# Kernel optimization log

Measured on AMD Instinct MI355X. Metric: run time of the kernel, lower is better.

The kernel has to match this reference:

```python
import jax, jax.numpy as jnp
import numpy as np

NEG_SLOPE = 0.2  # PyG GATConv leaky_relu slope


def gat_conv(x, src, dst, W, a_src, a_dst, bias, heads, out_ch, concat, n_nodes):
    # x: [N, in], W: [heads*out_ch, in], a_src/a_dst: [heads, out_ch]
    h = (x @ W.T).reshape(n_nodes, heads, out_ch)          # [N,H,C]
    alpha_src = (h * a_src).sum(-1)                         # [N,H]
    alpha_dst = (h * a_dst).sum(-1)                         # [N,H]
    e = jax.nn.leaky_relu(alpha_src[src] + alpha_dst[dst], NEG_SLOPE)  # [E,H]
    # segment softmax over incoming edges of each dst node (self-loops ensure non-empty)
    m = jax.ops.segment_max(e, dst, num_segments=n_nodes)
    e = jnp.exp(e - m[dst])
    s = jax.ops.segment_sum(e, dst, num_segments=n_nodes)
    alpha = e / (s[dst] + 1e-16)                            # [E,H]
    msg = h[src] * alpha[:, :, None]                        # [E,H,C]
    out = jax.ops.segment_sum(msg, dst, num_segments=n_nodes)  # [N,H,C]
    out = out.reshape(n_nodes, heads * out_ch) if concat else out.mean(axis=1)
    return out + bias


def setup_inputs() -> dict:
    key = jax.random.key(0)
    ks = jax.random.split(key, 16)
    N, E, IN, HID, OUT, H1, H2 = 10000, 160000, 256, 32, 32, 8, 10
    inp = {
        "x": jax.random.normal(ks[0], (N, IN), dtype=jnp.float32),
        "edge_index": jax.random.randint(ks[1], (2, E), 0, N, dtype=jnp.int64),
        # GATConv 1: in=256 -> 8 heads x 32
        "W1": jax.random.normal(ks[2], (H1 * HID, IN), dtype=jnp.float32) * 0.05,
        "a1s": jax.random.normal(ks[3], (H1, HID), dtype=jnp.float32) * 0.05,
        "a1d": jax.random.normal(ks[4], (H1, HID), dtype=jnp.float32) * 0.05,
        "b1": jnp.zeros((H1 * HID,), dtype=jnp.float32),
        # GATConv 2: in=256 -> 8 heads x 32
        "W2": jax.random.normal(ks[5], (H1 * HID, H1 * HID), dtype=jnp.float32) * 0.05,
        "a2s": jax.random.normal(ks[6], (H1, HID), dtype=jnp.float32) * 0.05,
        "a2d": jax.random.normal(ks[7], (H1, HID), dtype=jnp.float32) * 0.05,
        "b2": jnp.zeros((H1 * HID,), dtype=jnp.float32),
        # GATConv 3: in=256 -> 10 heads x 32, concat=False (mean)
        "W3": jax.random.normal(ks[8], (H2 * OUT, H1 * HID), dtype=jnp.float32) * 0.05,
        "a3s": jax.random.normal(ks[9], (H2, OUT), dtype=jnp.float32) * 0.05,
        "a3d": jax.random.normal(ks[10], (H2, OUT), dtype=jnp.float32) * 0.05,
        "b3": jnp.zeros((OUT,), dtype=jnp.float32),
        # residual projections
        "P1W": jax.random.normal(ks[11], (H1 * HID, IN), dtype=jnp.float32) * 0.05,
        "P1b": jnp.zeros((H1 * HID,), dtype=jnp.float32),
        "P3W": jax.random.normal(ks[12], (OUT, H1 * HID), dtype=jnp.float32) * 0.05,
        "P3b": jnp.zeros((OUT,), dtype=jnp.float32),
    }
    return inp


def reference(x, edge_index, W1, a1s, a1d, b1, W2, a2s, a2d, b2,
              W3, a3s, a3d, b3, P1W, P1b, P3W, P3b):
    N = x.shape[0]
    loop = jnp.arange(N, dtype=edge_index.dtype)
    src = jnp.concatenate([edge_index[0], loop])  # PyG adds self-loops by default
    dst = jnp.concatenate([edge_index[1], loop])

    identity1 = x @ P1W.T + P1b
    h = gat_conv(x, src, dst, W1, a1s, a1d, b1, 8, 32, True, N)
    h = jax.nn.elu(h) + identity1  # dropout inactive in eval

    identity2 = h
    h2 = gat_conv(h, src, dst, W2, a2s, a2d, b2, 8, 32, True, N)
    h = jax.nn.elu(h2) + identity2

    identity3 = h @ P3W.T + P3b
    h3 = gat_conv(h, src, dst, W3, a3s, a3d, b3, 10, 32, False, N)
    return h3 + identity3
```

## Files before the change

kernel.cpp:

```cpp
#include <hip/hip_runtime.h>
#include <hip/hip_bf16.h>

typedef __hip_bfloat16 bf16;
typedef __attribute__((ext_vector_type(8))) short bf16x8;
typedef __attribute__((ext_vector_type(4))) short bf16x4;
typedef __attribute__((ext_vector_type(4))) float f32x4;


static __device__ __forceinline__ float bf2f(bf16 v) { return __bfloat162float(v); }
static __device__ __forceinline__ float bf2fs(short v) {
    unsigned int u = ((unsigned int)(unsigned short)v) << 16;
    return __builtin_bit_cast(float, u);
}
static __device__ __forceinline__ short f2bfs(float f) {
    bf16 b = __float2bfloat16(f);
    return __builtin_bit_cast(short, b);
}
static __device__ __forceinline__ float loadf(const void* p, size_t i, int isf32) {
    return isf32 ? ((const float*)p)[i] : bf2f(((const bf16*)p)[i]);
}
static __device__ __forceinline__ int get_isf32(const int* flags) {
    return (flags[0] | (flags[2] == 0)) ? 1 : 0;
}
static __device__ __forceinline__ void wave_lds_fence() {
    asm volatile("s_waitcnt lgkmcnt(0)" ::: "memory");
}

__global__ void k_zero(int* __restrict__ flags, int* __restrict__ cnt, int N) {
    int i = blockIdx.x * blockDim.x + threadIdx.x;
    if (i < 4) flags[i] = 0;
    for (; i < N; i += gridDim.x * blockDim.x) cnt[i] = 0;
}

__global__ void k_detect(const unsigned short* __restrict__ xu, const int* __restrict__ ew,
                         int* __restrict__ flags, int nx, int ne2, int bx) {
    __shared__ int lf[3];
    if (threadIdx.x < 3) lf[threadIdx.x] = 0;
    __syncthreads();
    if ((int)blockIdx.x < bx) {
        for (int i = blockIdx.x * 256 + threadIdx.x; i < nx; i += bx * 256) {
            unsigned short v = xu[i];
            if ((v & 0x7F80u) == 0x7F80u) lf[0] = 1;
            if (((i & 1) == 0) && v != 0) lf[2] = 1;
        }
    } else {
        int nb = gridDim.x - bx;
        for (int i = (blockIdx.x - bx) * 256 + threadIdx.x; i < ne2; i += nb * 256) {
            if ((i & 1) && ew[i] != 0) lf[1] = 1;
        }
    }
    __syncthreads();
    if (threadIdx.x == 0) {
        if (lf[0]) atomicOr(&flags[0], 1);
        if (lf[1]) atomicOr(&flags[1], 1);
        if (lf[2]) atomicOr(&flags[2], 1);
    }
}

static __device__ __forceinline__ void cast8(const void* src, bf16* dst, int i8, int isf32) {
    if (isf32) {
        f32x4 a = ((const f32x4*)src)[2 * i8];
        f32x4 b = ((const f32x4*)src)[2 * i8 + 1];
        bf16x8 o;
        o[0] = f2bfs(a[0]); o[1] = f2bfs(a[1]); o[2] = f2bfs(a[2]); o[3] = f2bfs(a[3]);
        o[4] = f2bfs(b[0]); o[5] = f2bfs(b[1]); o[6] = f2bfs(b[2]); o[7] = f2bfs(b[3]);
        ((bf16x8*)dst)[i8] = o;
    } else {
        ((bf16x8*)dst)[i8] = ((const bf16x8*)src)[i8];
    }
}

__global__ void k_cast_norm(const void* s0, bf16* d0, int c0,
                            const void* s1, bf16* d1, int c1,
                            const void* s2, bf16* d2, int c2,
                            const void* s3, bf16* d3, int c3,
                            const void* s4, bf16* d4, int c4,
                            const void* s5, bf16* d5, int c5,
                            const int* __restrict__ w, int* __restrict__ es,
                            int* __restrict__ ed, int* __restrict__ cnt, int E,
                            const int* __restrict__ flags, int cb) {
    if ((int)blockIdx.x < cb) {
        int t = blockIdx.x * 256 + threadIdx.x;
        int isf32 = get_isf32(flags);
        if (t < c0) { if (isf32) cast8(s0, d0, t, 1); return; } t -= c0;
        if (t < c1) { cast8(s1, d1, t, isf32); return; } t -= c1;
        if (t < c2) { cast8(s2, d2, t, isf32); return; } t -= c2;
        if (t < c3) { cast8(s3, d3, t, isf32); return; } t -= c3;
        if (t < c4) { cast8(s4, d4, t, isf32); return; } t -= c4;
        if (t < c5) { cast8(s5, d5, t, isf32); }
    } else {
        int e = (blockIdx.x - cb) * 256 + threadIdx.x;
        if (e >= E) return;
        int sv, dv;
        if (flags[1] == 0) {
            sv = w[2 * (size_t)e];
            dv = w[2 * (size_t)E + 2 * (size_t)e];
        } else {
            sv = w[e];
            dv = w[(size_t)E + e];
        }
        es[e] = sv;
        ed[e] = dv;
        atomicAdd(&cnt[dv], 1);
    }
}

__global__ void k_scan(int* __restrict__ cnt, int* __restrict__ row_ptr, int N) {
    __shared__ int part[1024];
    int tid = threadIdx.x;
    int vpt = (N + 1023) >> 10;
    int i0 = tid * vpt;
    int i1 = i0 + vpt; if (i1 > N) i1 = N;
    int s = 0;
    for (int i = i0; i < i1; ++i) s += cnt[i] + 1;
    part[tid] = s;
    __syncthreads();
    for (int off = 1; off < 1024; off <<= 1) {
        int t = (tid >= off) ? part[tid - off] : 0;
        __syncthreads();
        part[tid] += t;
        __syncthreads();
    }
    int run = (tid == 0) ? 0 : part[tid - 1];
    for (int i = i0; i < i1; ++i) {
        int c = cnt[i] + 1;
        cnt[i] = run;
        run += c;
        row_ptr[i + 1] = run;
    }
    if (tid == 0) row_ptr[0] = 0;
}

__global__ void k_fill(const int* __restrict__ edst, int* __restrict__ cursor,
                       const int* __restrict__ row_ptr, int* __restrict__ csr_e,
                       int E, int N) {
    int e = blockIdx.x * blockDim.x + threadIdx.x;
    if (e < E) {
        int d = edst[e];
        int pos = atomicAdd(&cursor[d], 1);
        csr_e[pos] = e;
    } else if (e < E + N) {
        int d = e - E;
        csr_e[row_ptr[d + 1] - 1] = e;
    }
}

template<int NT, int KK>
__global__ void k_gemm_split(const bf16* __restrict__ Acast, const void* __restrict__ Araw,
                             const bf16* __restrict__ W,
                             const void* __restrict__ bias1, const int* __restrict__ flags,
                             bf16* __restrict__ out0, int S0, int ld0,
                             bf16* __restrict__ out1, int ld1, int n1,
                             int M, int Fo,
                             const void* __restrict__ aS, const void* __restrict__ aD,
                             float* __restrict__ asrc, float* __restrict__ adst, int H) {
    int wid = threadIdx.x >> 6;
    int lane = threadIdx.x & 63;
    int mrow = blockIdx.x * 64 + wid * 16;
    if (mrow >= M) return;
    int isf32 = get_isf32(flags);
    const bf16* A = (Araw && !isf32) ? (const bf16*)Araw : Acast;
    int ncol = blockIdx.y * (NT * 16);
    int r = lane & 15, g = lane >> 4;

    f32x4 acc[NT];
#pragma unroll
    for (int t = 0; t < NT; ++t) acc[t] = (f32x4){0.f, 0.f, 0.f, 0.f};

    const bf16* arow = A + (size_t)(mrow + r) * KK + g * 8;
    const bf16* wbase = W + (size_t)(ncol + r) * KK + g * 8;
#pragma unroll
    for (int k0 = 0; k0 < KK; k0 += 32) {
        bf16x8 af = *(const bf16x8*)(arow + k0);
#pragma unroll
        for (int t = 0; t < NT; ++t) {
            bf16x8 bfr = *(const bf16x8*)(wbase + (size_t)t * 16 * KK + k0);
            acc[t] = __builtin_amdgcn_mfma_f32_16x16x32_bf16(af, bfr, acc[t], 0, 0, 0);
        }
    }

#pragma unroll
    for (int t = 0; t < NT; ++t) {
        int n = ncol + t * 16 + r;
        bool is0 = n < S0;
        int jc = n - S0;
        float bv = (!is0 && jc < n1 && bias1) ? loadf(bias1, jc, isf32) : 0.f;
#pragma unroll
        for (int j = 0; j < 4; ++j) {
            int m = mrow + 4 * g + j;
            float v = acc[t][j] + bv;
            if (is0) out0[(size_t)m * ld0 + n] = __float2bfloat16(v);
            else if (jc < n1) out1[(size_t)m * ld1 + jc] = __float2bfloat16(v);
        }
    }

    if (aS && ncol < S0) {
        float ps[2][4], pd[2][4];
#pragma unroll
        for (int hb = 0; hb < 2; ++hb)
#pragma unroll
            for (int j = 0; j < 4; ++j) { ps[hb][j] = 0.f; pd[hb][j] = 0.f; }
#pragma unroll
        for (int t = 0; t < NT; ++t) {
            int col = ncol + t * 16 + r;
            float asv = loadf(aS, col, isf32);
            float adv = loadf(aD, col, isf32);
#pragma unroll
            for (int j = 0; j < 4; ++j) {
                ps[t >> 1][j] += acc[t][j] * asv;
                pd[t >> 1][j] += acc[t][j] * adv;
            }
        }
#pragma unroll
        for (int mk = 1; mk <= 8; mk <<= 1) {
#pragma unroll
            for (int hb = 0; hb < 2; ++hb)
#pragma unroll
                for (int j = 0; j < 4; ++j) {
                    ps[hb][j] += __shfl_xor(ps[hb][j], mk);
                    pd[hb][j] += __shfl_xor(pd[hb][j], mk);
                }
        }
        if (r == 0) {
            int hA = ncol >> 5, hB = hA + 1;
#pragma unroll
            for (int j = 0; j < 4; ++j) {
                int m = mrow + 4 * g + j;
                asrc[(size_t)m * H + hA] = ps[0][j];
                asrc[(size_t)m * H + hB] = ps[1][j];
                adst[(size_t)m * H + hA] = pd[0][j];
                adst[(size_t)m * H + hB] = pd[1][j];
            }
        }
    }
}

#define CAP 96
__global__ void k_fused_agg(const bf16* __restrict__ hlin,
                            const float* __restrict__ asrc, const float* __restrict__ adst,
                            const int* __restrict__ esrc, const int* __restrict__ row_ptr,
                            const int* __restrict__ csr_e,
                            const void* __restrict__ bias, const bf16* __restrict__ identb,
                            void* __restrict__ out, bf16* __restrict__ outb,
                            const int* __restrict__ flags,
                            int E, int N, int H, int mode) {
    __shared__ float el[4][CAP * 10];
    __shared__ int   ssrc[4][CAP];
    __shared__ float idn[4][10];
    int wid = threadIdx.x >> 6, lane = threadIdx.x & 63;
    int d = blockIdx.x * 4 + wid;
    bool active = d < N;
    int isf32 = get_isf32(flags);
    int F = H * 32;
    int nj = (F + 255) >> 8;
    int lo = 0, deg = 0;
    if (active) { lo = row_ptr[d]; deg = row_ptr[d + 1] - lo; }
    bool fast = deg <= CAP;
    if (!active) return;

    if (fast) {
        int EC = 64 / H;
        int h = lane % H, ei = lane / H;
        float ad = adst[(size_t)d * H + h];
        for (int base = 0; base < deg; base += EC) {
            int p = base + ei;
            if (ei < EC && p < deg) {
                int e = csr_e[lo + p];
                int s = (e < E) ? esrc[e] : (e - E);
                float v = asrc[(size_t)s * H + h] + ad;
                v = (v > 0.f) ? v : 0.2f * v;
                el[wid][p * H + h] = v;
                if (h == 0) ssrc[wid][p] = s;
            }
        }
    }
    wave_lds_fence();
    if (fast) {
        if (H == 8) {
            int h = lane & 7, sub = lane >> 3;
            float m = -1e30f;
            for (int p = sub; p < deg; p += 8) m = fmaxf(m, el[wid][p * 8 + h]);
            m = fmaxf(m, __shfl_xor(m, 8));
            m = fmaxf(m, __shfl_xor(m, 16));
            m = fmaxf(m, __shfl_xor(m, 32));
            float den = 0.f;
            for (int p = sub; p < deg; p += 8) {
                float t = __expf(el[wid][p * 8 + h] - m);
                el[wid][p * 8 + h] = t;
                den += t;
            }
            den += __shfl_xor(den, 8);
            den += __shfl_xor(den, 16);
            den += __shfl_xor(den, 32);
            if (lane < 8) idn[wid][lane] = 1.f / (den + 1e-16f);
        } else if (lane < H) {
            float m = -1e30f;
            for (int p = 0; p < deg; ++p) m = fmaxf(m, el[wid][p * H + lane]);
            float den = 0.f;
            for (int p = 0; p < deg; ++p) {
                float t = __expf(el[wid][p * H + lane] - m);
                el[wid][p * H + lane] = t;
                den += t;
            }
            idn[wid][lane] = 1.f / (den + 1e-16f);
        }
    }
    wave_lds_fence();

    if (mode == 1 && fast) {
        int g = lane & 15, q = lane >> 4;
        int f0 = g * 16;
        f32x4 a0 = {0.f,0.f,0.f,0.f}, a1 = {0.f,0.f,0.f,0.f};
        f32x4 a2 = {0.f,0.f,0.f,0.f}, a3 = {0.f,0.f,0.f,0.f};
        int p = q;
        for (; p + 4 < deg; p += 8) {
            int s0 = ssrc[wid][p];
            int s1 = ssrc[wid][p + 4];
            const bf16* hp0 = hlin + (size_t)s0 * 256 + f0;
            const bf16* hp1 = hlin + (size_t)s1 * 256 + f0;
            bf16x8 u0 = *(const bf16x8*)hp0;
            bf16x8 u1 = *(const bf16x8*)(hp0 + 8);
            bf16x8 v0 = *(const bf16x8*)hp1;
            bf16x8 v1 = *(const bf16x8*)(hp1 + 8);
            float w0 = el[wid][p * 8 + (g >> 1)];
            float w1 = el[wid][(p + 4) * 8 + (g >> 1)];
#pragma unroll
            for (int k = 0; k < 4; ++k) {
                a0[k] += w0 * bf2fs(u0[k]);
                a1[k] += w0 * bf2fs(u0[4 + k]);
                a2[k] += w0 * bf2fs(u1[k]);
                a3[k] += w0 * bf2fs(u1[4 + k]);
                a0[k] += w1 * bf2fs(v0[k]);
                a1[k] += w1 * bf2fs(v0[4 + k]);
                a2[k] += w1 * bf2fs(v1[k]);
                a3[k] += w1 * bf2fs(v1[4 + k]);
            }
        }
        if (p < deg) {
            int s0 = ssrc[wid][p];
            const bf16* hp0 = hlin + (size_t)s0 * 256 + f0;
            bf16x8 u0 = *(const bf16x8*)hp0;
            bf16x8 u1 = *(const bf16x8*)(hp0 + 8);
            float w0 = el[wid][p * 8 + (g >> 1)];
#pragma unroll
            for (int k = 0; k < 4; ++k) {
                a0[k] += w0 * bf2fs(u0[k]);
                a1[k] += w0 * bf2fs(u0[4 + k]);
                a2[k] += w0 * bf2fs(u1[k]);
                a3[k] += w0 * bf2fs(u1[4 + k]);
            }
        }
#pragma unroll
        for (int k = 0; k < 4; ++k) {
            a0[k] += __shfl_xor(a0[k], 16); a1[k] += __shfl_xor(a1[k], 16);
            a2[k] += __shfl_xor(a2[k], 16); a3[k] += __shfl_xor(a3[k], 16);
            a0[k] += __shfl_xor(a0[k], 32); a1[k] += __shfl_xor(a1[k], 32);
            a2[k] += __shfl_xor(a2[k], 32); a3[k] += __shfl_xor(a3[k], 32);
        }
        if (lane < 16) {
            float inv = idn[wid][g >> 1];
            const bf16* idp = identb + (size_t)d * 256 + f0;
            bf16x8 id0 = *(const bf16x8*)idp;
            bf16x8 id1 = *(const bf16x8*)(idp + 8);
            bf16* ob = outb + (size_t)d * 256 + f0;
            f32x4 av[4] = {a0, a1, a2, a3};
            bf16x8 obv0, obv1;
#pragma unroll
            for (int i = 0; i < 4; ++i) {
#pragma unroll
                for (int k = 0; k < 4; ++k) {
                    float v = av[i][k] * inv + loadf(bias, f0 + 4 * i + k, isf32);
                    v = (v > 0.f) ? v : (__expf(v) - 1.f);
                    int e8 = 4 * i + k;
                    v += bf2fs((e8 < 8) ? id0[e8] : id1[e8 - 8]);
                    if (i < 2) obv0[e8] = f2bfs(v);
                    else       obv1[e8 - 8] = f2bfs(v);
                }
            }
            *(bf16x8*)ob = obv0;
            *(bf16x8*)(ob + 8) = obv1;
        }
        return;
    }

    if (mode == 2 && fast) {
        int g = lane & 15, q = lane >> 4;
        int f0 = g * 16;
        int f1 = 256 + g * 4;
        f32x4 a0 = {0.f,0.f,0.f,0.f}, a1 = {0.f,0.f,0.f,0.f};
        f32x4 a2 = {0.f,0.f,0.f,0.f}, a3 = {0.f,0.f,0.f,0.f};
        f32x4 a4 = {0.f,0.f,0.f,0.f};
        int p = q;
        for (; p + 4 < deg; p += 8) {
            int s0 = ssrc[wid][p];
            int s1 = ssrc[wid][p + 4];
            const bf16* hp0 = hlin + (size_t)s0 * 320;
            const bf16* hp1 = hlin + (size_t)s1 * 320;
            bf16x8 u0 = *(const bf16x8*)(hp0 + f0);
            bf16x8 u1 = *(const bf16x8*)(hp0 + f0 + 8);
            bf16x4 u2 = *(const bf16x4*)(hp0 + f1);
            bf16x8 v0 = *(const bf16x8*)(hp1 + f0);
            bf16x8 v1 = *(const bf16x8*)(hp1 + f0 + 8);
            bf16x4 v2 = *(const bf16x4*)(hp1 + f1);
            float w00 = el[wid][p * 10 + (g >> 1)];
            float w02 = el[wid][p * 10 + 8 + (g >> 3)];
            float w10 = el[wid][(p + 4) * 10 + (g >> 1)];
            float w12 = el[wid][(p + 4) * 10 + 8 + (g >> 3)];
#pragma unroll
            for (int k = 0; k < 4; ++k) {
                a0[k] += w00 * bf2fs(u0[k]);
                a1[k] += w00 * bf2fs(u0[4 + k]);
                a2[k] += w00 * bf2fs(u1[k]);
                a3[k] += w00 * bf2fs(u1[4 + k]);
                a4[k] += w02 * bf2fs(u2[k]);
                a0[k] += w10 * bf2fs(v0[k]);
                a1[k] += w10 * bf2fs(v0[4 + k]);
                a2[k] += w10 * bf2fs(v1[k]);
                a3[k] += w10 * bf2fs(v1[4 + k]);
                a4[k] += w12 * bf2fs(v2[k]);
            }
        }
        if (p < deg) {
            int s0 = ssrc[wid][p];
            const bf16* hp0 = hlin + (size_t)s0 * 320;
            bf16x8 u0 = *(const bf16x8*)(hp0 + f0);
            bf16x8 u1 = *(const bf16x8*)(hp0 + f0 + 8);
            bf16x4 u2 = *(const bf16x4*)(hp0 + f1);
            float w00 = el[wid][p * 10 + (g >> 1)];
            float w02 = el[wid][p * 10 + 8 + (g >> 3)];
#pragma unroll
            for (int k = 0; k < 4; ++k) {
                a0[k] += w00 * bf2fs(u0[k]);
                a1[k] += w00 * bf2fs(u0[4 + k]);
                a2[k] += w00 * bf2fs(u1[k]);
                a3[k] += w00 * bf2fs(u1[4 + k]);
                a4[k] += w02 * bf2fs(u2[k]);
            }
        }
#pragma unroll
        for (int k = 0; k < 4; ++k) {
            a0[k] += __shfl_xor(a0[k], 16); a1[k] += __shfl_xor(a1[k], 16);
            a2[k] += __shfl_xor(a2[k], 16); a3[k] += __shfl_xor(a3[k], 16);
            a4[k] += __shfl_xor(a4[k], 16);
            a0[k] += __shfl_xor(a0[k], 32); a1[k] += __shfl_xor(a1[k], 32);
            a2[k] += __shfl_xor(a2[k], 32); a3[k] += __shfl_xor(a3[k], 32);
            a4[k] += __shfl_xor(a4[k], 32);
        }
        float* scratch = &el[wid][0];
        if (lane < 16) {
            float inv0 = idn[wid][g >> 1];
            float inv2 = idn[wid][8 + (g >> 3)];
#pragma unroll
            for (int k = 0; k < 4; ++k) {
                scratch[f0 + k]      = a0[k] * inv0;
                scratch[f0 + 4 + k]  = a1[k] * inv0;
                scratch[f0 + 8 + k]  = a2[k] * inv0;
                scratch[f0 + 12 + k] = a3[k] * inv0;
                scratch[f1 + k]      = a4[k] * inv2;
            }
        }
        wave_lds_fence();
        if (lane < 32) {
            float s = 0.f;
#pragma unroll
            for (int h = 0; h < 10; ++h) s += scratch[h * 32 + lane];
            float v = s * 0.1f + loadf(bias, lane, isf32)
                    + bf2f(identb[(size_t)d * 32 + lane]);
            if (isf32) ((float*)out)[(size_t)d * 32 + lane] = v;
            else ((bf16*)out)[(size_t)d * 32 + lane] = __float2bfloat16(v);
        }
        return;
    }

    f32x4 acc[2] = {(f32x4){0.f,0.f,0.f,0.f}, (f32x4){0.f,0.f,0.f,0.f}};
    for (int j = 0; j < nj; ++j) {
        int f0 = (lane + 64 * j) * 4;
        if (f0 >= F) continue;
        int hj = f0 >> 5;
        float ad = adst[(size_t)d * H + hj];
        float m = -1e30f;
        for (int p = 0; p < deg; ++p) {
            int e = csr_e[lo + p];
            int s = (e < E) ? esrc[e] : (e - E);
            float v = asrc[(size_t)s * H + hj] + ad;
            v = (v > 0.f) ? v : 0.2f * v;
            m = fmaxf(m, v);
        }
        float den = 0.f;
        f32x4 a4 = {0.f, 0.f, 0.f, 0.f};
        for (int p = 0; p < deg; ++p) {
            int e = csr_e[lo + p];
            int s = (e < E) ? esrc[e] : (e - E);
            float v = asrc[(size_t)s * H + hj] + ad;
            v = (v > 0.f) ? v : 0.2f * v;
            float t = __expf(v - m);
            den += t;
            bf16x4 hv = *(const bf16x4*)(hlin + (size_t)s * F + f0);
            for (int k = 0; k < 4; ++k) a4[k] += t * bf2fs(hv[k]);
        }
        float inv = 1.f / (den + 1e-16f);
        for (int k = 0; k < 4; ++k) acc[j][k] = a4[k] * inv;
    }
    if (mode == 1) {
        int f0 = lane * 4;
        bf16x4 ob;
#pragma unroll
        for (int k = 0; k < 4; ++k) {
            float v = acc[0][k] + loadf(bias, f0 + k, isf32);
            v = (v > 0.f) ? v : (__expf(v) - 1.f);
            v += bf2f(identb[(size_t)d * F + f0 + k]);
            ob[k] = f2bfs(v);
        }
        *(bf16x4*)(outb + (size_t)d * F + f0) = ob;
    } else {
        float* scratch = &el[wid][0];
#pragma unroll
        for (int j = 0; j < 2; ++j) {
            int f0 = (lane + 64 * j) * 4;
            if (j < nj && f0 < F) {
#pragma unroll
                for (int k = 0; k < 4; ++k) scratch[f0 + k] = acc[j][k];
            }
        }
        wave_lds_fence();
        if (lane < 32) {
            float s = 0.f;
            for (int h = 0; h < H; ++h) s += scratch[h * 32 + lane];
            float v = s * (1.f / (float)H) + loadf(bias, lane, isf32)
                    + bf2f(identb[(size_t)d * 32 + lane]);
            if (isf32) ((float*)out)[(size_t)d * 32 + lane] = v;
            else ((bf16*)out)[(size_t)d * 32 + lane] = __float2bfloat16(v);
        }
    }
}

extern "C" void kernel_launch(void* const* d_in, const int* in_sizes, int n_in,
                              void* d_out, int out_size, void* d_ws, size_t ws_size,
                              hipStream_t stream) {
    const int IN = 256, C = 32;
    const int N = in_sizes[0] / IN;
    const int E = in_sizes[1] / 2;
    const int ET = E + N;

    const void* x    = d_in[0];
    const int*  edge = (const int*)d_in[1];
    const void* W1 = d_in[2];
    const void* a1s = d_in[3];
    const void* a1d = d_in[4];
    const void* b1 = d_in[5];
    const void* W2 = d_in[6];
    const void* a2s = d_in[7];
    const void* a2d = d_in[8];
    const void* b2 = d_in[9];
    const void* W3 = d_in[10];
    const void* a3s = d_in[11];
    const void* a3d = d_in[12];
    const void* b3 = d_in[13];
    const void* P1W = d_in[14];
    const void* P1b = d_in[15];
    const void* P3W = d_in[16];
    const void* P3b = d_in[17];

    char* ws = (char*)d_ws;
    size_t off = 0;
    auto alloc = [&](size_t bytes) -> void* {
        void* p = ws + off;
        off = (off + bytes + 255) & ~(size_t)255;
        return p;
    };
    bf16* fxb   = (bf16*)alloc((size_t)N * 256 * 2);
    bf16* fyb   = (bf16*)alloc((size_t)N * 256 * 2);
    bf16* fhb   = (bf16*)alloc((size_t)N * 320 * 2);
    bf16* fidb  = (bf16*)alloc((size_t)N * 256 * 2);
    float* fasrc = (float*)alloc((size_t)N * 10 * 4);
    float* fadst = (float*)alloc((size_t)N * 10 * 4);
    bf16* wc1   = (bf16*)alloc((size_t)512 * 256 * 2);
    bf16* wb2   = (bf16*)alloc((size_t)256 * 256 * 2);
    bf16* wc3   = (bf16*)alloc((size_t)384 * 256 * 2);
    int*  isrc  = (int*)alloc((size_t)E * 4);
    int*  idst  = (int*)alloc((size_t)E * 4);
    int*  irow  = (int*)alloc((size_t)(N + 1) * 4);
    int*  icur  = (int*)alloc((size_t)N * 4);
    int*  icsr  = (int*)alloc((size_t)ET * 4);
    int*  flags = (int*)alloc(4 * 4);
    (void)ws_size;

    auto cdiv = [](int a, int b) { return (a + b - 1) / b; };

    k_zero<<<cdiv(N, 256), 256, 0, stream>>>(flags, icur, N);

    int nprobe_x = (N * 256 < 16384) ? N * 256 : 16384;
    int nprobe_e = (2 * E < 8192) ? 2 * E : 8192;
    int bx = cdiv(nprobe_x, 256) < 16 ? cdiv(nprobe_x, 256) : 16;
    int be = cdiv(nprobe_e, 256) < 8 ? cdiv(nprobe_e, 256) : 8;
    k_detect<<<bx + be, 256, 0, stream>>>(
        (const unsigned short*)x, edge, flags, nprobe_x, nprobe_e, bx);

    int c_x = N * 256 / 8, c_w = 256 * 256 / 8, c_w3 = 320 * 256 / 8, c_p3 = 32 * 256 / 8;
    int ctot = c_x + 3 * c_w + c_w3 + c_p3;
    int cb = cdiv(ctot, 256);
    k_cast_norm<<<cb + cdiv(E, 256), 256, 0, stream>>>(
        x, fxb, c_x,
        W1, wc1, c_w,
        P1W, wc1 + (size_t)256 * 256, c_w,
        W2, wb2, c_w,
        W3, wc3, c_w3,
        P3W, wc3 + (size_t)320 * 256, c_p3,
        edge, isrc, idst, icur, E, flags, cb);

    k_scan<<<1, 1024, 0, stream>>>(icur, irow, N);
    k_fill<<<cdiv(ET, 256), 256, 0, stream>>>(idst, icur, irow, icsr, E, N);

    int gx = cdiv(N, 64);
    int ga = cdiv(N, 4);

    {
        int H = 8;
        k_gemm_split<4, 256><<<dim3(gx, 8), 256, 0, stream>>>(
            fxb, x, wc1, P1b, flags, fhb, 256, 256, fidb, 256, 256, N, 512,
            a1s, a1d, fasrc, fadst, H);
        k_fused_agg<<<ga, 256, 0, stream>>>(fhb, fasrc, fadst, isrc, irow, icsr,
                                            b1, fidb, nullptr, fyb, flags, E, N, H, 1);
    }
    {
        int H = 8;
        k_gemm_split<4, 256><<<dim3(gx, 4), 256, 0, stream>>>(
            fyb, nullptr, wb2, nullptr, flags, fhb, 256, 256, nullptr, 0, 0, N, 256,
            a2s, a2d, fasrc, fadst, H);
        k_fused_agg<<<ga, 256, 0, stream>>>(fhb, fasrc, fadst, isrc, irow, icsr,
                                            b2, fyb, nullptr, fyb, flags, E, N, H, 1);
    }
    {
        int H = 10;
        k_gemm_split<4, 256><<<dim3(gx, 6), 256, 0, stream>>>(
            fyb, nullptr, wc3, P3b, flags, fhb, 320, 320, fidb, 32, 32, N, 384,
            a3s, a3d, fasrc, fadst, H);
        k_fused_agg<<<ga, 256, 0, stream>>>(fhb, fasrc, fadst, isrc, irow, icsr,
                                            b3, fidb, d_out, nullptr, flags, E, N, H, 2);
    }
}
```

Before: 199.2 us.

## Widen GEMM column tile to 128 and read bf16 weights directly

Each GEMM block now covers 8 MFMA column tiles instead of 4, which halves the grid's y dimension and lets each A fragment be reused across twice as many columns. Weights are read through per-tile pointers into separate segment buffers, so bf16 inputs are used directly without a copy and the cast kernel exits early when the inputs are not fp32. The attention-score epilogue is generalized to handle more heads per block, with a boundary guard for the layer 3 split. The trade-off is higher register pressure from 8 accumulators and 8 weight pointers, plus fewer blocks in flight.

```diff
diff --git a/kernel.cpp b/kernel.cpp
--- a/kernel.cpp
+++ b/kernel.cpp
@@ -57,17 +57,13 @@
     }
 }
 
-static __device__ __forceinline__ void cast8(const void* src, bf16* dst, int i8, int isf32) {
-    if (isf32) {
-        f32x4 a = ((const f32x4*)src)[2 * i8];
-        f32x4 b = ((const f32x4*)src)[2 * i8 + 1];
-        bf16x8 o;
-        o[0] = f2bfs(a[0]); o[1] = f2bfs(a[1]); o[2] = f2bfs(a[2]); o[3] = f2bfs(a[3]);
-        o[4] = f2bfs(b[0]); o[5] = f2bfs(b[1]); o[6] = f2bfs(b[2]); o[7] = f2bfs(b[3]);
-        ((bf16x8*)dst)[i8] = o;
-    } else {
-        ((bf16x8*)dst)[i8] = ((const bf16x8*)src)[i8];
-    }
+static __device__ __forceinline__ void cast8(const void* src, bf16* dst, int i8) {
+    f32x4 a = ((const f32x4*)src)[2 * i8];
+    f32x4 b = ((const f32x4*)src)[2 * i8 + 1];
+    bf16x8 o;
+    o[0] = f2bfs(a[0]); o[1] = f2bfs(a[1]); o[2] = f2bfs(a[2]); o[3] = f2bfs(a[3]);
+    o[4] = f2bfs(b[0]); o[5] = f2bfs(b[1]); o[6] = f2bfs(b[2]); o[7] = f2bfs(b[3]);
+    ((bf16x8*)dst)[i8] = o;
 }
 
 __global__ void k_cast_norm(const void* s0, bf16* d0, int c0,
@@ -80,14 +76,14 @@
                             int* __restrict__ ed, int* __restrict__ cnt, int E,
                             const int* __restrict__ flags, int cb) {
     if ((int)blockIdx.x < cb) {
+        if (!get_isf32(flags)) return;
         int t = blockIdx.x * 256 + threadIdx.x;
-        int isf32 = get_isf32(flags);
-        if (t < c0) { if (isf32) cast8(s0, d0, t, 1); return; } t -= c0;
-        if (t < c1) { cast8(s1, d1, t, isf32); return; } t -= c1;
-        if (t < c2) { cast8(s2, d2, t, isf32); return; } t -= c2;
-        if (t < c3) { cast8(s3, d3, t, isf32); return; } t -= c3;
-        if (t < c4) { cast8(s4, d4, t, isf32); return; } t -= c4;
-        if (t < c5) { cast8(s5, d5, t, isf32); }
+        if (t < c0) { cast8(s0, d0, t); return; } t -= c0;
+        if (t < c1) { cast8(s1, d1, t); return; } t -= c1;
+        if (t < c2) { cast8(s2, d2, t); return; } t -= c2;
+        if (t < c3) { cast8(s3, d3, t); return; } t -= c3;
+        if (t < c4) { cast8(s4, d4, t); return; } t -= c4;
+        if (t < c5) { cast8(s5, d5, t); }
     } else {
         int e = (blockIdx.x - cb) * 256 + threadIdx.x;
         if (e >= E) return;
@@ -146,14 +142,16 @@
 }
 
 template<int NT, int KK>
-__global__ void k_gemm_split(const bf16* __restrict__ Acast, const void* __restrict__ Araw,
-                             const bf16* __restrict__ W,
-                             const void* __restrict__ bias1, const int* __restrict__ flags,
-                             bf16* __restrict__ out0, int S0, int ld0,
-                             bf16* __restrict__ out1, int ld1, int n1,
-                             int M, int Fo,
-                             const void* __restrict__ aS, const void* __restrict__ aD,
-                             float* __restrict__ asrc, float* __restrict__ adst, int H) {
+__global__ __launch_bounds__(256) void k_gemm_split(
+        const bf16* __restrict__ Acast, const void* __restrict__ Araw,
+        const void* __restrict__ W0raw, const bf16* __restrict__ W0cast, int S0,
+        const void* __restrict__ W1raw, const bf16* __restrict__ W1cast, int n1,
+        const void* __restrict__ bias1, const int* __restrict__ flags,
+        bf16* __restrict__ out0, int ld0,
+        bf16* __restrict__ out1, int ld1,
+        int M,
+        const void* __restrict__ aS, const void* __restrict__ aD,
+        float* __restrict__ asrc, float* __restrict__ adst, int H) {
     int wid = threadIdx.x >> 6;
     int lane = threadIdx.x & 63;
     int mrow = blockIdx.x * 64 + wid * 16;
@@ -163,18 +161,29 @@
     int ncol = blockIdx.y * (NT * 16);
     int r = lane & 15, g = lane >> 4;
 
+    const bf16* wptr[NT];
+#pragma unroll
+    for (int t = 0; t < NT; ++t) {
+        int nl = ncol + t * 16 + r;
+        bool is0 = nl < S0;
+        int jc = nl - S0;
+        int wr = is0 ? nl : ((jc < n1) ? jc : (n1 > 0 ? n1 - 1 : 0));
+        const bf16* wseg = is0 ? (isf32 ? W0cast : (const bf16*)W0raw)
+                               : (isf32 ? W1cast : (const bf16*)W1raw);
+        wptr[t] = wseg + (size_t)wr * KK + g * 8;
+    }
+
     f32x4 acc[NT];
 #pragma unroll
     for (int t = 0; t < NT; ++t) acc[t] = (f32x4){0.f, 0.f, 0.f, 0.f};
 
     const bf16* arow = A + (size_t)(mrow + r) * KK + g * 8;
-    const bf16* wbase = W + (size_t)(ncol + r) * KK + g * 8;
-#pragma unroll
+#pragma unroll 2
     for (int k0 = 0; k0 < KK; k0 += 32) {
         bf16x8 af = *(const bf16x8*)(arow + k0);
 #pragma unroll
         for (int t = 0; t < NT; ++t) {
-            bf16x8 bfr = *(const bf16x8*)(wbase + (size_t)t * 16 * KK + k0);
+            bf16x8 bfr = *(const bf16x8*)(wptr[t] + k0);
             acc[t] = __builtin_amdgcn_mfma_f32_16x16x32_bf16(af, bfr, acc[t], 0, 0, 0);
         }
     }
@@ -195,26 +204,28 @@
     }
 
     if (aS && ncol < S0) {
-        float ps[2][4], pd[2][4];
-#pragma unroll
-        for (int hb = 0; hb < 2; ++hb)
+        float ps[NT / 2][4], pd[NT / 2][4];
+#pragma unroll
+        for (int hb = 0; hb < NT / 2; ++hb)
 #pragma unroll
             for (int j = 0; j < 4; ++j) { ps[hb][j] = 0.f; pd[hb][j] = 0.f; }
 #pragma unroll
         for (int t = 0; t < NT; ++t) {
             int col = ncol + t * 16 + r;
-            float asv = loadf(aS, col, isf32);
-            float adv = loadf(aD, col, isf32);
-#pragma unroll
-            for (int j = 0; j < 4; ++j) {
-                ps[t >> 1][j] += acc[t][j] * asv;
-                pd[t >> 1][j] += acc[t][j] * adv;
+            if (col < S0) {
+                float asv = loadf(aS, col, isf32);
+                float adv = loadf(aD, col, isf32);
+#pragma unroll
+                for (int j = 0; j < 4; ++j) {
+                    ps[t >> 1][j] += acc[t][j] * asv;
+                    pd[t >> 1][j] += acc[t][j] * adv;
+                }
             }
         }
 #pragma unroll
         for (int mk = 1; mk <= 8; mk <<= 1) {
 #pragma unroll
-            for (int hb = 0; hb < 2; ++hb)
+            for (int hb = 0; hb < NT / 2; ++hb)
 #pragma unroll
                 for (int j = 0; j < 4; ++j) {
                     ps[hb][j] += __shfl_xor(ps[hb][j], mk);
@@ -222,14 +233,17 @@
                 }
         }
         if (r == 0) {
-            int hA = ncol >> 5, hB = hA + 1;
-#pragma unroll
-            for (int j = 0; j < 4; ++j) {
-                int m = mrow + 4 * g + j;
-                asrc[(size_t)m * H + hA] = ps[0][j];
-                asrc[(size_t)m * H + hB] = ps[1][j];
-                adst[(size_t)m * H + hA] = pd[0][j];
-                adst[(size_t)m * H + hB] = pd[1][j];
+#pragma unroll
+            for (int hb = 0; hb < NT / 2; ++hb) {
+                if (ncol + hb * 32 < S0) {
+                    int hA = (ncol >> 5) + hb;
+#pragma unroll
+                    for (int j = 0; j < 4; ++j) {
+                        int m = mrow + 4 * g + j;
+                        asrc[(size_t)m * H + hA] = ps[hb][j];
+                        adst[(size_t)m * H + hA] = pd[hb][j];
+                    }
+                }
             }
         }
     }
@@ -574,9 +588,11 @@
     bf16* fidb  = (bf16*)alloc((size_t)N * 256 * 2);
     float* fasrc = (float*)alloc((size_t)N * 10 * 4);
     float* fadst = (float*)alloc((size_t)N * 10 * 4);
-    bf16* wc1   = (bf16*)alloc((size_t)512 * 256 * 2);
-    bf16* wb2   = (bf16*)alloc((size_t)256 * 256 * 2);
-    bf16* wc3   = (bf16*)alloc((size_t)384 * 256 * 2);
+    bf16* wb1c  = (bf16*)alloc((size_t)256 * 256 * 2);
+    bf16* wbP1c = (bf16*)alloc((size_t)256 * 256 * 2);
+    bf16* wb2c  = (bf16*)alloc((size_t)256 * 256 * 2);
+    bf16* wb3c  = (bf16*)alloc((size_t)320 * 256 * 2);
+    bf16* wbP3c = (bf16*)alloc((size_t)32 * 256 * 2);
     int*  isrc  = (int*)alloc((size_t)E * 4);
     int*  idst  = (int*)alloc((size_t)E * 4);
     int*  irow  = (int*)alloc((size_t)(N + 1) * 4);
@@ -601,11 +617,11 @@
     int cb = cdiv(ctot, 256);
     k_cast_norm<<<cb + cdiv(E, 256), 256, 0, stream>>>(
         x, fxb, c_x,
-        W1, wc1, c_w,
-        P1W, wc1 + (size_t)256 * 256, c_w,
-        W2, wb2, c_w,
-        W3, wc3, c_w3,
-        P3W, wc3 + (size_t)320 * 256, c_p3,
+        W1, wb1c, c_w,
+        P1W, wbP1c, c_w,
+        W2, wb2c, c_w,
+        W3, wb3c, c_w3,
+        P3W, wbP3c, c_p3,
         edge, isrc, idst, icur, E, flags, cb);
 
     k_scan<<<1, 1024, 0, stream>>>(icur, irow, N);
@@ -616,24 +632,36 @@
 
     {
         int H = 8;
-        k_gemm_split<4, 256><<<dim3(gx, 8), 256, 0, stream>>>(
-            fxb, x, wc1, P1b, flags, fhb, 256, 256, fidb, 256, 256, N, 512,
+        k_gemm_split<8, 256><<<dim3(gx, 4), 256, 0, stream>>>(
+            fxb, x,
+            W1, wb1c, 256,
+            P1W, wbP1c, 256,
+            P1b, flags,
+            fhb, 256, fidb, 256, N,
             a1s, a1d, fasrc, fadst, H);
         k_fused_agg<<<ga, 256, 0, stream>>>(fhb, fasrc, fadst, isrc, irow, icsr,
                                             b1, fidb, nullptr, fyb, flags, E, N, H, 1);
     }
     {
         int H = 8;
-        k_gemm_split<4, 256><<<dim3(gx, 4), 256, 0, stream>>>(
-            fyb, nullptr, wb2, nullptr, flags, fhb, 256, 256, nullptr, 0, 0, N, 256,
+        k_gemm_split<8, 256><<<dim3(gx, 2), 256, 0, stream>>>(
+            fyb, nullptr,
+            W2, wb2c, 256,
+            nullptr, nullptr, 0,
+            nullptr, flags,
+            fhb, 256, nullptr, 0, N,
             a2s, a2d, fasrc, fadst, H);
         k_fused_agg<<<ga, 256, 0, stream>>>(fhb, fasrc, fadst, isrc, irow, icsr,
                                             b2, fyb, nullptr, fyb, flags, E, N, H, 1);
     }
     {
         int H = 10;
-        k_gemm_split<4, 256><<<dim3(gx, 6), 256, 0, stream>>>(
-            fyb, nullptr, wc3, P3b, flags, fhb, 320, 320, fidb, 32, 32, N, 384,
+        k_gemm_split<8, 256><<<dim3(gx, 3), 256, 0, stream>>>(
+            fyb, nullptr,
+            W3, wb3c, 320,
+            P3W, wbP3c, 32,
+            P3b, flags,
+            fhb, 320, fidb, 32, N,
             a3s, a3d, fasrc, fadst, H);
         k_fused_agg<<<ga, 256, 0, stream>>>(fhb, fasrc, fadst, isrc, irow, icsr,
                                             b3, fidb, d_out, nullptr, flags, E, N, H, 2);
```

Measured after the change: 214.3 us. +7.6%, slower.
